# Performance work log

Hardware: AMD Instinct MI355X
Metric: run time of the kernel (lower is better)

Reference implementation:

```python
import jax, jax.numpy as jnp
import numpy as np

NUM_EXPERTS = 8
TOP_K = 2

def setup_inputs() -> dict:
    key = jax.random.key(0)
    ks = jax.random.split(key, 6)
    B, S, D, H, E = 4, 2048, 1024, 4096, NUM_EXPERTS
    sc_g = 1.0 / np.sqrt(D)
    sc_1 = 1.0 / np.sqrt(D)
    sc_2 = 1.0 / np.sqrt(H)
    return {
        "x": jax.random.normal(ks[0], (B, S, D), dtype=jnp.float32),
        "Wg": jax.random.normal(ks[1], (D, E), dtype=jnp.float32) * sc_g,
        "W1": jax.random.normal(ks[2], (E, D, H), dtype=jnp.float32) * sc_1,
        "b1": jnp.zeros((E, H), dtype=jnp.float32),
        "W2": jax.random.normal(ks[3], (E, H, D), dtype=jnp.float32) * sc_2,
        "b2": jnp.zeros((E, D), dtype=jnp.float32),
    }

def reference(x, Wg, W1, b1, W2, b2):
    B, S, D = x.shape
    E = Wg.shape[1]
    T = B * S
    xf = x.reshape(T, D)

    # ---- Router (SparseRouter) ----
    logits = xf @ Wg                      # [T, E]
    probs = jax.nn.softmax(logits, axis=-1)
    w, idx = jax.lax.top_k(probs, TOP_K)  # [T, K]
    w = w / jnp.sum(w, axis=-1, keepdims=True)

    rows = jnp.arange(T)[:, None]
    # combine[t,e] = sum_k w[t,k] * 1[idx[t,k]==e]  (dispatch/combine weights)
    combine = jnp.zeros((T, E), dtype=xf.dtype).at[rows, idx].add(w)
    # load-balancing aux loss
    counts = jnp.zeros((T, E), dtype=xf.dtype).at[rows, idx].add(1.0)
    f_i = counts.mean(axis=0)
    p_i = probs.mean(axis=0)
    aux_loss = E * jnp.sum(f_i * p_i)

    # ---- Experts (ExpertFFN, dropout=identity in eval) ----
    h = jnp.einsum('td,edh->teh', xf, W1) + b1[None]      # [T, E, H]
    h = jax.nn.gelu(h, approximate=False)                  # torch GELU (exact erf)
    y = jnp.einsum('teh,ehd->ted', h, W2) + b2[None]       # [T, E, D]

    out = jnp.einsum('te,ted->td', combine, y).reshape(B, S, D)
    return (out, aux_loss)
```

## Files before the change

kernel.cpp:

```cpp
#include <hip/hip_runtime.h>
#include <hip/hip_bf16.h>
#include <math.h>

#define TTOK 8192
#define DDIM 1024
#define HDIM 4096
#define NEXP 8
#define BMT 256
#define MAXT 72
#define MAXSLOTS (MAXT * BMT)

typedef __bf16 bf16x8 __attribute__((ext_vector_type(8)));
typedef float f32x4 __attribute__((ext_vector_type(4)));
typedef const void __attribute__((address_space(1))) *gvp_t;
typedef void __attribute__((address_space(3))) *lvp_t;

__device__ __forceinline__ void gload16(const void *g, void *l) {
  __builtin_amdgcn_global_load_lds((gvp_t)g, (lvp_t)l, 16, 0, 0);
}


__global__ __launch_bounds__(64) void zero_meta(int *counts, int *cursors, float *probsum) {
  int i = threadIdx.x;
  if (i < NEXP) { counts[i] = 0; cursors[i] = 0; probsum[i] = 0.f; }
}

__global__ __launch_bounds__(256) void convert_x(const float *__restrict__ x,
                                                 __hip_bfloat16 *__restrict__ xb) {
  size_t i = ((size_t)blockIdx.x * 256 + threadIdx.x) * 4;
  float4 v = *(const float4 *)(x + i);
  union { __hip_bfloat16 h[4]; uint2 u; } p;
  p.h[0] = __float2bfloat16(v.x);
  p.h[1] = __float2bfloat16(v.y);
  p.h[2] = __float2bfloat16(v.z);
  p.h[3] = __float2bfloat16(v.w);
  *(uint2 *)(xb + i) = p.u;
}

__global__ __launch_bounds__(256) void transpose_cvt(const float *__restrict__ src,
                                                     __hip_bfloat16 *__restrict__ dst,
                                                     int R, int C) {
  __shared__ float tile[64][65];
  const int e = blockIdx.z;
  const int rb = blockIdx.x * 64, cb = blockIdx.y * 64;
  const size_t base = (size_t)e * R * C;
  const int lx = threadIdx.x & 63, ly = threadIdx.x >> 6;
#pragma unroll
  for (int i = 0; i < 64; i += 4)
    tile[ly + i][lx] = src[base + (size_t)(rb + ly + i) * C + cb + lx];
  __syncthreads();
#pragma unroll
  for (int i = 0; i < 64; i += 4)
    dst[base + (size_t)(cb + ly + i) * R + rb + lx] = __float2bfloat16(tile[lx][ly + i]);
}

__global__ __launch_bounds__(256) void router_k(const float *__restrict__ x,
                                                const float *__restrict__ Wg,
                                                int *__restrict__ counts,
                                                float *__restrict__ probsum,
                                                int *__restrict__ tok_e,
                                                float *__restrict__ tok_w) {
  __shared__ float sprob[NEXP];
  __shared__ int scnt[NEXP];
  if (threadIdx.x < NEXP) { sprob[threadIdx.x] = 0.f; scnt[threadIdx.x] = 0; }
  __syncthreads();

  const int wid = threadIdx.x >> 6, lane = threadIdx.x & 63;
  const int t = blockIdx.x * 4 + wid;
  const float *xr = x + (size_t)t * DDIM;
  double acc[NEXP];
#pragma unroll
  for (int e = 0; e < NEXP; ++e) acc[e] = 0.0;
  for (int j = lane; j < DDIM; j += 64) {
    double xv = (double)xr[j];
    const float *wrow = Wg + j * NEXP;
#pragma unroll
    for (int e = 0; e < NEXP; ++e) acc[e] += xv * (double)wrow[e];
  }
#pragma unroll
  for (int e = 0; e < NEXP; ++e) {
#pragma unroll
    for (int off = 32; off > 0; off >>= 1) acc[e] += __shfl_xor(acc[e], off, 64);
  }
  if (lane == 0) {
    double mx = acc[0];
    for (int e = 1; e < NEXP; ++e) mx = acc[e] > mx ? acc[e] : mx;
    double p[NEXP], s = 0.0;
    for (int e = 0; e < NEXP; ++e) { p[e] = exp(acc[e] - mx); s += p[e]; }
    for (int e = 0; e < NEXP; ++e) p[e] /= s;
    int i0 = 0;
    for (int e = 1; e < NEXP; ++e) if (p[e] > p[i0]) i0 = e;
    int i1 = (i0 == 0) ? 1 : 0;
    for (int e = 0; e < NEXP; ++e) if (e != i0 && p[e] > p[i1]) i1 = e;
    tok_e[t] = i0 | (i1 << 16);
    tok_w[t] = (float)(p[i0] / (p[i0] + p[i1]));
    atomicAdd(&scnt[i0], 1);
    atomicAdd(&scnt[i1], 1);
    for (int e = 0; e < NEXP; ++e) atomicAdd(&sprob[e], (float)p[e]);
  }
  __syncthreads();
  if (threadIdx.x < NEXP) {
    atomicAdd(&counts[threadIdx.x], scnt[threadIdx.x]);
    atomicAdd(&probsum[threadIdx.x], sprob[threadIdx.x]);
  }
}

__global__ __launch_bounds__(256) void offsets_k(const int *__restrict__ counts,
                                                 int *__restrict__ padoff,
                                                 int *__restrict__ tileexp,
                                                 int *__restrict__ total,
                                                 int *__restrict__ slot_tok,
                                                 float *__restrict__ slot_w) {
  __shared__ int sp[NEXP + 1];
  if (threadIdx.x == 0) {
    int off = 0, tt = 0;
    for (int e = 0; e < NEXP; ++e) {
      sp[e] = off;
      padoff[e] = off;
      int nt = (counts[e] + BMT - 1) >> 8;
      for (int i = 0; i < nt; ++i) tileexp[tt + i] = e;
      tt += nt;
      off += nt << 8;
    }
    sp[NEXP] = off;
    *total = tt;
  }
  __syncthreads();
  for (int e = 0; e < NEXP; ++e) {
    int s0 = sp[e] + counts[e], s1 = sp[e + 1];
    for (int s = s0 + (int)threadIdx.x; s < s1; s += 256) {
      slot_tok[s] = 0;
      slot_w[s] = 0.f;
    }
  }
}

__global__ __launch_bounds__(256) void assign_k(const int *__restrict__ tok_e,
                                                const float *__restrict__ tok_w,
                                                const int *__restrict__ padoff,
                                                int *__restrict__ cursors,
                                                int *__restrict__ slot_tok,
                                                float *__restrict__ slot_w,
                                                int *__restrict__ slot_of) {
  const int t = blockIdx.x * 256 + threadIdx.x;
  const int ee = tok_e[t];
  const int e0 = ee & 0xffff, e1 = ee >> 16;
  const float w0 = tok_w[t];
  int p0 = atomicAdd(&cursors[e0], 1);
  int s0 = padoff[e0] + p0;
  slot_tok[s0] = t; slot_w[s0] = w0; slot_of[2 * t] = s0;
  int p1 = atomicAdd(&cursors[e1], 1);
  int s1 = padoff[e1] + p1;
  slot_tok[s1] = t; slot_w[s1] = 1.0f - w0; slot_of[2 * t + 1] = s1;
}

template <int KD_, int ND_, bool GELU_, bool GATHER_>
__global__ __launch_bounds__(256, 3) void moe_97(
    const __hip_bfloat16 *__restrict__ A, const __hip_bfloat16 *__restrict__ Bw,
    const float *__restrict__ bias, __hip_bfloat16 *__restrict__ Cout,
    const int *__restrict__ slot_token, const int *__restrict__ tile_expert,
    const int *__restrict__ total_tiles) {
  constexpr int nkt = KD_ / 64;
  __shared__ __align__(16) char lsA[128 * 128];
  __shared__ __align__(16) char lsB[128 * 128];

  const int nbx = gridDim.x;
  const int fid = blockIdx.y * nbx + blockIdx.x;
  const int q8 = (nbx * gridDim.y) >> 3;
  const int rid = (fid & 7) * q8 + (fid >> 3);
  const int tile = rid % nbx;
  const int ncol = (rid / nbx) * 128;
  if (tile >= ((*total_tiles) << 1)) return;
  const int e = tile_expert[tile >> 1];

  const int tid = threadIdx.x;
  const int wid = tid >> 6, lane = tid & 63;
  const int sr = tid >> 3;
  const int scs = (((tid & 7) ^ (sr & 7)) * 8);
  const __hip_bfloat16 *Bb = Bw + (size_t)e * ((size_t)ND_ * KD_);
  const __hip_bfloat16 *ap[4], *bp[4];
#pragma unroll
  for (int c = 0; c < 4; ++c) {
    int r = tile * 128 + c * 32 + sr;
    int row = GATHER_ ? slot_token[r] : r;
    ap[c] = A + (size_t)row * KD_ + scs;
    bp[c] = Bb + (size_t)(ncol + c * 32 + sr) * KD_ + scs;
  }

  const int wr = wid >> 1, wc = wid & 1;
  const int ln15 = lane & 15, g4 = lane >> 4;
  int xsl[2];
#pragma unroll
  for (int kc = 0; kc < 2; ++kc) xsl[kc] = ((kc * 4 + g4) ^ (ln15 & 7)) << 4;
  const int abase = (wr * 64 + ln15) * 128;
  const int bbase = (wc * 64 + ln15) * 128;

  auto STAGE = [&](int kt) {
#pragma unroll
    for (int c = 0; c < 4; ++c) {
      gload16(ap[c] + kt * 64, lsA + c * 4096 + tid * 16);
      gload16(bp[c] + kt * 64, lsB + c * 4096 + tid * 16);
    }
  };

  f32x4 acc[4][4] = {};

  asm volatile("s_waitcnt vmcnt(0)" ::: "memory");
  STAGE(0);

  for (int kt = 0; kt < nkt; ++kt) {
    asm volatile("s_waitcnt vmcnt(0)" ::: "memory");
    __builtin_amdgcn_s_barrier();

    bf16x8 ar[4][2], br[4][2];
#pragma unroll
    for (int mi = 0; mi < 4; ++mi)
#pragma unroll
      for (int kc = 0; kc < 2; ++kc)
        ar[mi][kc] = *(const bf16x8 *)(lsA + abase + mi * 2048 + xsl[kc]);
#pragma unroll
    for (int nf = 0; nf < 4; ++nf)
#pragma unroll
      for (int kc = 0; kc < 2; ++kc)
        br[nf][kc] = *(const bf16x8 *)(lsB + bbase + nf * 2048 + xsl[kc]);

    asm volatile("s_waitcnt lgkmcnt(0)" ::: "memory");
    __builtin_amdgcn_sched_barrier(0);
    __builtin_amdgcn_s_barrier();

    if (kt + 1 < nkt) STAGE(kt + 1);
    __builtin_amdgcn_sched_barrier(0);

#pragma unroll
    for (int mi = 0; mi < 4; ++mi)
#pragma unroll
      for (int nf = 0; nf < 4; ++nf) {
        acc[mi][nf] = __builtin_amdgcn_mfma_f32_16x16x32_bf16(ar[mi][0], br[nf][0],
                                                              acc[mi][nf], 0, 0, 0);
        acc[mi][nf] = __builtin_amdgcn_mfma_f32_16x16x32_bf16(ar[mi][1], br[nf][1],
                                                              acc[mi][nf], 0, 0, 0);
      }
  }

  const float *be = bias + (size_t)e * ND_;
  const int colb = ncol + wc * 64 + ln15;
  float bv[4];
#pragma unroll
  for (int nf = 0; nf < 4; ++nf) bv[nf] = be[colb + nf * 16];
#pragma unroll
  for (int mi = 0; mi < 4; ++mi) {
    const int row0 = tile * 128 + wr * 64 + mi * 16 + g4 * 4;
#pragma unroll
    for (int nf = 0; nf < 4; ++nf) {
      const int col = colb + nf * 16;
#pragma unroll
      for (int r = 0; r < 4; ++r) {
        float v = acc[mi][nf][r] + bv[nf];
        if constexpr (GELU_) v = 0.5f * v * (1.0f + erff(v * 0.70710678118654752f));
        Cout[(size_t)(row0 + r) * ND_ + col] = __float2bfloat16(v);
      }
    }
  }
}

__global__ __launch_bounds__(256) void combine_k(const __hip_bfloat16 *__restrict__ yb,
                                                 const int *__restrict__ slot_of,
                                                 const float *__restrict__ slot_w,
                                                 float *__restrict__ out) {
  const int t = blockIdx.x;
  const int s0 = slot_of[2 * t], s1 = slot_of[2 * t + 1];
  const float w0 = slot_w[s0], w1 = slot_w[s1];
  const unsigned short *y = (const unsigned short *)yb;
  const int c = threadIdx.x * 4;
  ushort4 a = *(const ushort4 *)(y + (size_t)s0 * DDIM + c);
  ushort4 b = *(const ushort4 *)(y + (size_t)s1 * DDIM + c);
  float4 r;
  r.x = w0 * __uint_as_float((unsigned)a.x << 16) + w1 * __uint_as_float((unsigned)b.x << 16);
  r.y = w0 * __uint_as_float((unsigned)a.y << 16) + w1 * __uint_as_float((unsigned)b.y << 16);
  r.z = w0 * __uint_as_float((unsigned)a.z << 16) + w1 * __uint_as_float((unsigned)b.z << 16);
  r.w = w0 * __uint_as_float((unsigned)a.w << 16) + w1 * __uint_as_float((unsigned)b.w << 16);
  *(float4 *)(out + (size_t)t * DDIM + c) = r;
}

__global__ __launch_bounds__(64) void aux_k(const int *__restrict__ counts,
                                            const float *__restrict__ probsum,
                                            float *__restrict__ outp) {
  if (threadIdx.x == 0) {
    double s = 0.0;
    for (int e = 0; e < NEXP; ++e)
      s += ((double)counts[e] / (double)TTOK) * ((double)probsum[e] / (double)TTOK);
    *outp = (float)((double)NEXP * s);
  }
}

extern "C" void kernel_launch(void *const *d_in, const int *in_sizes, int n_in,
                              void *d_out, int out_size, void *d_ws, size_t ws_size,
                              hipStream_t stream) {
  const float *x  = (const float *)d_in[0];
  const float *Wg = (const float *)d_in[1];
  const float *W1 = (const float *)d_in[2];
  const float *b1 = (const float *)d_in[3];
  const float *W2 = (const float *)d_in[4];
  const float *b2 = (const float *)d_in[5];
  float *out = (float *)d_out;

  char *ws = (char *)d_ws;
  const size_t MB = 1ull << 20;
  int   *counts   = (int *)(ws + 0);
  int   *cursors  = (int *)(ws + 64);
  int   *padoff   = (int *)(ws + 128);
  int   *tileexp  = (int *)(ws + 192);
  int   *total    = (int *)(ws + 768);
  float *probsum  = (float *)(ws + 832);
  int   *tok_e    = (int *)(ws + 4096);
  float *tok_w    = (float *)(ws + 36864);
  int   *slot_tok = (int *)(ws + 69632);
  float *slot_w   = (float *)(ws + 147456);
  int   *slot_of  = (int *)(ws + 225280);
  __hip_bfloat16 *xb  = (__hip_bfloat16 *)(ws + 1 * MB);
  __hip_bfloat16 *w1t = (__hip_bfloat16 *)(ws + 17 * MB);
  __hip_bfloat16 *hb  = (__hip_bfloat16 *)(ws + 81 * MB);
  __hip_bfloat16 *w2t = (__hip_bfloat16 *)(ws + 1 * MB);
  __hip_bfloat16 *yb  = (__hip_bfloat16 *)(ws + 225 * MB);

  zero_meta<<<1, 64, 0, stream>>>(counts, cursors, probsum);
  convert_x<<<8192, 256, 0, stream>>>(x, xb);
  transpose_cvt<<<dim3(16, 64, 8), 256, 0, stream>>>(W1, w1t, DDIM, HDIM);
  router_k<<<TTOK / 4, 256, 0, stream>>>(x, Wg, counts, probsum, tok_e, tok_w);
  offsets_k<<<1, 256, 0, stream>>>(counts, padoff, tileexp, total, slot_tok, slot_w);
  assign_k<<<TTOK / 256, 256, 0, stream>>>(tok_e, tok_w, padoff, cursors, slot_tok, slot_w, slot_of);
  moe_97<DDIM, HDIM, true, true><<<dim3(2 * MAXT, HDIM / 128), 256, 0, stream>>>(
      xb, w1t, b1, hb, slot_tok, tileexp, total);
  transpose_cvt<<<dim3(64, 16, 8), 256, 0, stream>>>(W2, w2t, HDIM, DDIM);
  moe_97<HDIM, DDIM, false, false><<<dim3(2 * MAXT, DDIM / 128), 256, 0, stream>>>(
      hb, w2t, b2, yb, slot_tok, tileexp, total);
  combine_k<<<TTOK, 256, 0, stream>>>(yb, slot_of, slot_w, out);
  aux_k<<<1, 64, 0, stream>>>(counts, probsum, out + (size_t)TTOK * DDIM);
}
```

Before: 601.1 us.

## Fuse x conversion into router, fold aux loss into offsets, fast GELU, unroll GEMM K loop

The fp32-to-bf16 conversion of x now happens inside the router kernel, which reads x with float4 loads, removing one pass over x and one launch. The aux-loss computation moves into offsets_k, dropping another single-thread launch. The GEMM K loop is unrolled in blocks of eight steps with a compile-time prefetch schedule, and exact erf GELU is replaced by the Abramowitz-Stegun polynomial approximation using hardware rcp and exp2. The GELU approximation has an absolute error around 1e-7 and could slightly change outputs, and the unrolled loop increases code size.

```diff
diff --git a/kernel.cpp b/kernel.cpp
--- a/kernel.cpp
+++ b/kernel.cpp
@@ -19,22 +19,25 @@
   __builtin_amdgcn_global_load_lds((gvp_t)g, (lvp_t)l, 16, 0, 0);
 }
 
+__device__ __forceinline__ float gelu_f(float v) {
+  const float z = v * 0.70710678118654752f;
+  const float az = fabsf(z);
+  const float t = __builtin_amdgcn_rcpf(fmaf(0.3275911f, az, 1.0f));
+  float p = fmaf(1.061405429f, t, -1.453152027f);
+  p = fmaf(p, t, 1.421413741f);
+  p = fmaf(p, t, -0.284496736f);
+  p = fmaf(p, t, 0.254829592f);
+  p *= t;
+  const float ez = __builtin_amdgcn_exp2f(az * az * -1.4426950408889634f);
+  float r = fmaf(-p, ez, 1.0f);
+  r = (v < 0.f) ? -r : r;
+  return 0.5f * v * (1.0f + r);
+}
+
 
 __global__ __launch_bounds__(64) void zero_meta(int *counts, int *cursors, float *probsum) {
   int i = threadIdx.x;
   if (i < NEXP) { counts[i] = 0; cursors[i] = 0; probsum[i] = 0.f; }
-}
-
-__global__ __launch_bounds__(256) void convert_x(const float *__restrict__ x,
-                                                 __hip_bfloat16 *__restrict__ xb) {
-  size_t i = ((size_t)blockIdx.x * 256 + threadIdx.x) * 4;
-  float4 v = *(const float4 *)(x + i);
-  union { __hip_bfloat16 h[4]; uint2 u; } p;
-  p.h[0] = __float2bfloat16(v.x);
-  p.h[1] = __float2bfloat16(v.y);
-  p.h[2] = __float2bfloat16(v.z);
-  p.h[3] = __float2bfloat16(v.w);
-  *(uint2 *)(xb + i) = p.u;
 }
 
 __global__ __launch_bounds__(256) void transpose_cvt(const float *__restrict__ src,
@@ -59,7 +62,8 @@
                                                 int *__restrict__ counts,
                                                 float *__restrict__ probsum,
                                                 int *__restrict__ tok_e,
-                                                float *__restrict__ tok_w) {
+                                                float *__restrict__ tok_w,
+                                                __hip_bfloat16 *__restrict__ xb) {
   __shared__ float sprob[NEXP];
   __shared__ int scnt[NEXP];
   if (threadIdx.x < NEXP) { sprob[threadIdx.x] = 0.f; scnt[threadIdx.x] = 0; }
@@ -68,14 +72,26 @@
   const int wid = threadIdx.x >> 6, lane = threadIdx.x & 63;
   const int t = blockIdx.x * 4 + wid;
   const float *xr = x + (size_t)t * DDIM;
+  __hip_bfloat16 *xbr = xb + (size_t)t * DDIM;
   double acc[NEXP];
 #pragma unroll
   for (int e = 0; e < NEXP; ++e) acc[e] = 0.0;
-  for (int j = lane; j < DDIM; j += 64) {
-    double xv = (double)xr[j];
-    const float *wrow = Wg + j * NEXP;
-#pragma unroll
-    for (int e = 0; e < NEXP; ++e) acc[e] += xv * (double)wrow[e];
+#pragma unroll
+  for (int it = 0; it < DDIM / 256; ++it) {
+    const int j = it * 256 + lane * 4;
+    float4 v = *(const float4 *)(xr + j);
+    float vv[4] = {v.x, v.y, v.z, v.w};
+    union { __hip_bfloat16 h[4]; uint2 u; } pk;
+#pragma unroll
+    for (int u = 0; u < 4; ++u) pk.h[u] = __float2bfloat16(vv[u]);
+    *(uint2 *)(xbr + j) = pk.u;
+    const float *w0 = Wg + (size_t)j * NEXP;
+#pragma unroll
+    for (int u = 0; u < 4; ++u) {
+      double xv = (double)vv[u];
+#pragma unroll
+      for (int e = 0; e < NEXP; ++e) acc[e] += xv * (double)w0[u * NEXP + e];
+    }
   }
 #pragma unroll
   for (int e = 0; e < NEXP; ++e) {
@@ -106,15 +122,19 @@
 }
 
 __global__ __launch_bounds__(256) void offsets_k(const int *__restrict__ counts,
+                                                 const float *__restrict__ probsum,
                                                  int *__restrict__ padoff,
                                                  int *__restrict__ tileexp,
                                                  int *__restrict__ total,
                                                  int *__restrict__ slot_tok,
-                                                 float *__restrict__ slot_w) {
+                                                 float *__restrict__ slot_w,
+                                                 float *__restrict__ aux_out) {
   __shared__ int sp[NEXP + 1];
   if (threadIdx.x == 0) {
     int off = 0, tt = 0;
+    double s = 0.0;
     for (int e = 0; e < NEXP; ++e) {
+      s += ((double)counts[e] / (double)TTOK) * ((double)probsum[e] / (double)TTOK);
       sp[e] = off;
       padoff[e] = off;
       int nt = (counts[e] + BMT - 1) >> 8;
@@ -124,6 +144,7 @@
     }
     sp[NEXP] = off;
     *total = tt;
+    *aux_out = (float)((double)NEXP * s);
   }
   __syncthreads();
   for (int e = 0; e < NEXP; ++e) {
@@ -161,6 +182,8 @@
     const int *__restrict__ slot_token, const int *__restrict__ tile_expert,
     const int *__restrict__ total_tiles) {
   constexpr int nkt = KD_ / 64;
+  constexpr int NB = nkt / 8;
+  static_assert(nkt % 8 == 0, "K must be multiple of 512");
   __shared__ __align__(16) char lsA[128 * 128];
   __shared__ __align__(16) char lsB[128 * 128];
 
@@ -186,6 +209,7 @@
     ap[c] = A + (size_t)row * KD_ + scs;
     bp[c] = Bb + (size_t)(ncol + c * 32 + sr) * KD_ + scs;
   }
+  const int tid16 = tid * 16;
 
   const int wr = wid >> 1, wc = wid & 1;
   const int ln15 = lane & 15, g4 = lane >> 4;
@@ -195,51 +219,67 @@
   const int abase = (wr * 64 + ln15) * 128;
   const int bbase = (wc * 64 + ln15) * 128;
 
-  auto STAGE = [&](int kt) {
-#pragma unroll
-    for (int c = 0; c < 4; ++c) {
-      gload16(ap[c] + kt * 64, lsA + c * 4096 + tid * 16);
-      gload16(bp[c] + kt * 64, lsB + c * 4096 + tid * 16);
-    }
-  };
-
   f32x4 acc[4][4] = {};
 
   asm volatile("s_waitcnt vmcnt(0)" ::: "memory");
-  STAGE(0);
-
-  for (int kt = 0; kt < nkt; ++kt) {
-    asm volatile("s_waitcnt vmcnt(0)" ::: "memory");
-    __builtin_amdgcn_s_barrier();
-
-    bf16x8 ar[4][2], br[4][2];
-#pragma unroll
-    for (int mi = 0; mi < 4; ++mi)
-#pragma unroll
-      for (int kc = 0; kc < 2; ++kc)
-        ar[mi][kc] = *(const bf16x8 *)(lsA + abase + mi * 2048 + xsl[kc]);
-#pragma unroll
-    for (int nf = 0; nf < 4; ++nf)
-#pragma unroll
-      for (int kc = 0; kc < 2; ++kc)
-        br[nf][kc] = *(const bf16x8 *)(lsB + bbase + nf * 2048 + xsl[kc]);
-
-    asm volatile("s_waitcnt lgkmcnt(0)" ::: "memory");
-    __builtin_amdgcn_sched_barrier(0);
-    __builtin_amdgcn_s_barrier();
-
-    if (kt + 1 < nkt) STAGE(kt + 1);
-    __builtin_amdgcn_sched_barrier(0);
-
-#pragma unroll
-    for (int mi = 0; mi < 4; ++mi)
-#pragma unroll
-      for (int nf = 0; nf < 4; ++nf) {
-        acc[mi][nf] = __builtin_amdgcn_mfma_f32_16x16x32_bf16(ar[mi][0], br[nf][0],
-                                                              acc[mi][nf], 0, 0, 0);
-        acc[mi][nf] = __builtin_amdgcn_mfma_f32_16x16x32_bf16(ar[mi][1], br[nf][1],
-                                                              acc[mi][nf], 0, 0, 0);
+#pragma unroll
+  for (int c = 0; c < 4; ++c) {
+    gload16(ap[c], lsA + c * 4096 + tid16);
+    gload16(bp[c], lsB + c * 4096 + tid16);
+  }
+
+  for (int kb = 0; kb < NB; ++kb) {
+    const bool more = (kb + 1 < NB);
+#pragma unroll
+    for (int j = 0; j < 8; ++j) {
+      asm volatile("s_waitcnt vmcnt(0)" ::: "memory");
+      __builtin_amdgcn_s_barrier();
+
+      bf16x8 ar[4][2], br[4][2];
+#pragma unroll
+      for (int mi = 0; mi < 4; ++mi)
+#pragma unroll
+        for (int kc = 0; kc < 2; ++kc)
+          ar[mi][kc] = *(const bf16x8 *)(lsA + abase + mi * 2048 + xsl[kc]);
+#pragma unroll
+      for (int nf = 0; nf < 4; ++nf)
+#pragma unroll
+        for (int kc = 0; kc < 2; ++kc)
+          br[nf][kc] = *(const bf16x8 *)(lsB + bbase + nf * 2048 + xsl[kc]);
+
+      asm volatile("s_waitcnt lgkmcnt(0)" ::: "memory");
+      __builtin_amdgcn_sched_barrier(0);
+      __builtin_amdgcn_s_barrier();
+
+      if (j < 7) {
+#pragma unroll
+        for (int c = 0; c < 4; ++c) {
+          gload16(ap[c] + (j + 1) * 64, lsA + c * 4096 + tid16);
+          gload16(bp[c] + (j + 1) * 64, lsB + c * 4096 + tid16);
+        }
+      } else {
+#pragma unroll
+        for (int c = 0; c < 4; ++c) { ap[c] += 512; bp[c] += 512; }
+        if (more) {
+#pragma unroll
+          for (int c = 0; c < 4; ++c) {
+            gload16(ap[c], lsA + c * 4096 + tid16);
+            gload16(bp[c], lsB + c * 4096 + tid16);
+          }
+        }
       }
+      __builtin_amdgcn_sched_barrier(0);
+
+#pragma unroll
+      for (int mi = 0; mi < 4; ++mi)
+#pragma unroll
+        for (int nf = 0; nf < 4; ++nf) {
+          acc[mi][nf] = __builtin_amdgcn_mfma_f32_16x16x32_bf16(
+              ar[mi][0], br[nf][0], acc[mi][nf], 0, 0, 0);
+          acc[mi][nf] = __builtin_amdgcn_mfma_f32_16x16x32_bf16(
+              ar[mi][1], br[nf][1], acc[mi][nf], 0, 0, 0);
+        }
+    }
   }
 
   const float *be = bias + (size_t)e * ND_;
@@ -256,7 +296,7 @@
 #pragma unroll
       for (int r = 0; r < 4; ++r) {
         float v = acc[mi][nf][r] + bv[nf];
-        if constexpr (GELU_) v = 0.5f * v * (1.0f + erff(v * 0.70710678118654752f));
+        if constexpr (GELU_) v = gelu_f(v);
         Cout[(size_t)(row0 + r) * ND_ + col] = __float2bfloat16(v);
       }
     }
@@ -280,17 +320,6 @@
   r.z = w0 * __uint_as_float((unsigned)a.z << 16) + w1 * __uint_as_float((unsigned)b.z << 16);
   r.w = w0 * __uint_as_float((unsigned)a.w << 16) + w1 * __uint_as_float((unsigned)b.w << 16);
   *(float4 *)(out + (size_t)t * DDIM + c) = r;
-}
-
-__global__ __launch_bounds__(64) void aux_k(const int *__restrict__ counts,
-                                            const float *__restrict__ probsum,
-                                            float *__restrict__ outp) {
-  if (threadIdx.x == 0) {
-    double s = 0.0;
-    for (int e = 0; e < NEXP; ++e)
-      s += ((double)counts[e] / (double)TTOK) * ((double)probsum[e] / (double)TTOK);
-    *outp = (float)((double)NEXP * s);
-  }
 }
 
 extern "C" void kernel_launch(void *const *d_in, const int *in_sizes, int n_in,
@@ -324,10 +353,10 @@
   __hip_bfloat16 *yb  = (__hip_bfloat16 *)(ws + 225 * MB);
 
   zero_meta<<<1, 64, 0, stream>>>(counts, cursors, probsum);
-  convert_x<<<8192, 256, 0, stream>>>(x, xb);
+  router_k<<<TTOK / 4, 256, 0, stream>>>(x, Wg, counts, probsum, tok_e, tok_w, xb);
   transpose_cvt<<<dim3(16, 64, 8), 256, 0, stream>>>(W1, w1t, DDIM, HDIM);
-  router_k<<<TTOK / 4, 256, 0, stream>>>(x, Wg, counts, probsum, tok_e, tok_w);
-  offsets_k<<<1, 256, 0, stream>>>(counts, padoff, tileexp, total, slot_tok, slot_w);
+  offsets_k<<<1, 256, 0, stream>>>(counts, probsum, padoff, tileexp, total,
+                                   slot_tok, slot_w, out + (size_t)TTOK * DDIM);
   assign_k<<<TTOK / 256, 256, 0, stream>>>(tok_e, tok_w, padoff, cursors, slot_tok, slot_w, slot_of);
   moe_97<DDIM, HDIM, true, true><<<dim3(2 * MAXT, HDIM / 128), 256, 0, stream>>>(
       xb, w1t, b1, hb, slot_tok, tileexp, total);
@@ -335,5 +364,4 @@
   moe_97<HDIM, DDIM, false, false><<<dim3(2 * MAXT, DDIM / 128), 256, 0, stream>>>(
       hb, w2t, b2, yb, slot_tok, tileexp, total);
   combine_k<<<TTOK, 256, 0, stream>>>(yb, slot_of, slot_w, out);
-  aux_k<<<1, 64, 0, stream>>>(counts, probsum, out + (size_t)TTOK * DDIM);
-}
+}
```

Measured after the change: 771.7 us. 1.28x slower.
